# Kernel optimization log

Measured on AMD Instinct MI355X. Metric: run time of the kernel, lower is better.

The kernel has to match this reference:

```python
import jax, jax.numpy as jnp
import numpy as np

HIDDEN = 1024
HEADS = 16
HEAD_DIM = HIDDEN // HEADS
B, T = 4, 2048


def setup_inputs() -> dict:
    key = jax.random.key(0)
    k_x, k_w1, k_b1, k_w2, k_b2 = jax.random.split(key, 5)
    lim1 = 1.0 / np.sqrt(HIDDEN)
    x = jax.random.normal(k_x, (B, T, HIDDEN), dtype=jnp.float32)
    # causal lower-triangular mask, broadcastable to [B, H, T, T]
    mask = jnp.tril(jnp.ones((T, T), dtype=jnp.int32))[None, None, :, :]
    # qkv_proj: Linear(HIDDEN, 3*HIDDEN); torch Linear: y = x @ W.T + b
    W_qkv = jax.random.uniform(k_w1, (3 * HIDDEN, HIDDEN), minval=-lim1, maxval=lim1, dtype=jnp.float32)
    b_qkv = jax.random.uniform(k_b1, (3 * HIDDEN,), minval=-lim1, maxval=lim1, dtype=jnp.float32)
    W_out = jax.random.uniform(k_w2, (HIDDEN, HIDDEN), minval=-lim1, maxval=lim1, dtype=jnp.float32)
    b_out = jax.random.uniform(k_b2, (HIDDEN,), minval=-lim1, maxval=lim1, dtype=jnp.float32)
    return {"x": x, "mask": mask, "W_qkv": W_qkv, "b_qkv": b_qkv, "W_out": W_out, "b_out": b_out}


def reference(x, mask, W_qkv, b_qkv, W_out, b_out):
    Bx, Tx, C = x.shape
    qkv = x @ W_qkv.T + b_qkv                      # [B, T, 3C]
    qkv = qkv.reshape(Bx, Tx, 3, HEADS, HEAD_DIM)
    qkv = jnp.transpose(qkv, (2, 0, 3, 1, 4))      # [3, B, H, T, Dh]
    Q, K, V = qkv[0], qkv[1], qkv[2]
    scale = 1.0 / np.sqrt(HEAD_DIM)
    scores = jnp.einsum('bhqd,bhkd->bhqk', Q, K) * scale  # [B, H, T, T]
    scores = jnp.where(mask == 0, -jnp.inf, scores)
    probs = jax.nn.softmax(scores, axis=-1)
    ctx = jnp.einsum('bhqk,bhkd->bhqd', probs, V)  # [B, H, T, Dh]
    ctx = jnp.transpose(ctx, (0, 2, 1, 3)).reshape(Bx, Tx, C)
    return ctx @ W_out.T + b_out
```

## Files before the change

### kernel.cpp

```cpp
#include <hip/hip_runtime.h>
#include <cstdint>
#include <cstddef>

#define B_ 4
#define T_ 2048
#define C_ 1024
#define H_ 16
#define D_ 64

typedef __attribute__((ext_vector_type(8))) __bf16 bf16x8;
typedef __attribute__((ext_vector_type(4))) float floatx4;

#define QSCL (0.125f * 1.44269504088896f)
#define FMAX 24.0f

__device__ __forceinline__ unsigned short f2bf(float f) {
  union { float f; unsigned int u; } v; v.f = f;
  unsigned int r = v.u + 0x7fffu + ((v.u >> 16) & 1u);
  return (unsigned short)(r >> 16);
}
__device__ __forceinline__ ushort4 pk4(float a, float b, float c, float d) {
  ushort4 u; u.x = f2bf(a); u.y = f2bf(b); u.z = f2bf(c); u.w = f2bf(d);
  return u;
}
__device__ __forceinline__ bf16x8 cvt8(float4 a, float4 b) {
  bf16x8 r;
  r[0] = a.x; r[1] = a.y; r[2] = a.z; r[3] = a.w;
  r[4] = b.x; r[5] = b.y; r[6] = b.z; r[7] = b.w;
  return r;
}
__device__ __forceinline__ unsigned pkbf2(float a, float b) {
  union { __bf16 h[2]; unsigned u; } w;
  w.h[0] = (__bf16)a; w.h[1] = (__bf16)b;
  return w.u;
}

__device__ __forceinline__ void gl_lds16(const void* g, void* l) {
  __builtin_amdgcn_global_load_lds(
      (const __attribute__((address_space(1))) unsigned int*)g,
      (__attribute__((address_space(3))) unsigned int*)l, 16, 0, 0);
}

__global__ __launch_bounds__(256)
void conv_bf16(const float* __restrict__ src, unsigned short* __restrict__ dst,
               int n8) {
  for (int i = blockIdx.x * 256 + threadIdx.x; i < n8; i += gridDim.x * 256) {
    const float4* s = (const float4*)src + 2 * (size_t)i;
    float4 a = s[0], b = s[1];
    ((bf16x8*)dst)[i] = cvt8(a, b);
  }
}

__global__ __launch_bounds__(256)
void conv_tri(const float* __restrict__ s1, unsigned short* __restrict__ d1, int n1,
              const float* __restrict__ s2, unsigned short* __restrict__ d2, int n2,
              const float* __restrict__ s3, unsigned short* __restrict__ d3, int n3) {
  for (int i = blockIdx.x * 256 + threadIdx.x; i < n1 + n2 + n3; i += gridDim.x * 256) {
    const float4* sp; bf16x8* dp;
    if (i < n1)           { sp = (const float4*)s1 + 2 * (size_t)i;       dp = (bf16x8*)d1 + i; }
    else if (i < n1 + n2) { int j = i - n1;      sp = (const float4*)s2 + 2 * (size_t)j; dp = (bf16x8*)d2 + j; }
    else                  { int j = i - n1 - n2; sp = (const float4*)s3 + 2 * (size_t)j; dp = (bf16x8*)d3 + j; }
    float4 a = sp[0], b = sp[1];
    *dp = cvt8(a, b);
  }
}

template<int EPI, int GATHER, int WBF>
__global__ __launch_bounds__(256, 3)
void gemm_bt(const unsigned short* __restrict__ Abf,
             const void* __restrict__ Wraw,
             const float* __restrict__ bias,
             float* __restrict__ out,
             unsigned short* __restrict__ qws,
             unsigned short* __restrict__ kws,
             unsigned short* __restrict__ vtws)
{
  alignas(16) __shared__ unsigned short As[128 * 64];
  alignas(16) __shared__ unsigned short Bs[WBF ? 128 * 64 : 128 * 72];
  const int tid  = threadIdx.x;
  const int lane = tid & 63;
  const int wid  = tid >> 6;
  const int col  = lane & 15;
  const int quad = lane >> 4;
  const int wm = (wid >> 1) << 6;
  const int wn = (wid & 1) << 6;
  const int bm = blockIdx.y << 7;
  const int bn = blockIdx.x << 7;

  const float* Wf          = (const float*)Wraw;
  const unsigned short* Wb = (const unsigned short*)Wraw;

  const int r0 = tid >> 3;
  const int c0 = tid & 7;

  floatx4 acc[4][4];
#pragma unroll
  for (int i = 0; i < 4; ++i)
#pragma unroll
    for (int j = 0; j < 4; ++j)
      acc[i][j] = (floatx4){0.f, 0.f, 0.f, 0.f};

  for (int k0 = 0; k0 < 1024; k0 += 64) {
    __syncthreads();
#pragma unroll
    for (int s = 0; s < 4; ++s) {
      const int row  = (s << 5) + r0;
      const int colE = ((c0 ^ (row & 7)) << 3);
      const unsigned short* gsrc;
      if (GATHER) {
        const int m = bm + row;
        const int b = m >> 11, t = m & 2047;
        const int h = k0 >> 6;
        gsrc = Abf + ((((size_t)(b * 16 + h) << 11) + t) << 6) + colE;
      } else {
        gsrc = Abf + (size_t)(bm + row) * 1024 + k0 + colE;
      }
      gl_lds16(gsrc, (char*)As + (s << 12) + (wid << 10));
    }
    if (WBF) {
#pragma unroll
      for (int s = 0; s < 4; ++s) {
        const int row  = (s << 5) + r0;
        const int colE = ((c0 ^ (row & 7)) << 3);
        const unsigned short* gsrc = Wb + (size_t)(bn + row) * 1024 + k0 + colE;
        gl_lds16(gsrc, (char*)Bs + (s << 12) + (wid << 10));
      }
    } else {
#pragma unroll
      for (int s = 0; s < 4; ++s) {
        const int row = (s << 5) + r0;
        const int kc  = c0 << 3;
        const float* wsrc = &Wf[(size_t)(bn + row) * 1024 + k0 + kc];
        float4 w0 = *(const float4*)wsrc;
        float4 w1 = *(const float4*)(wsrc + 4);
        *(bf16x8*)&Bs[row * 72 + kc] = cvt8(w0, w1);
      }
    }
    __syncthreads();
#pragma unroll
    for (int kk = 0; kk < 64; kk += 32) {
      bf16x8 af[4], bfr[4];
#pragma unroll
      for (int i = 0; i < 4; ++i) {
        const int r = wm + i * 16 + col;
        af[i] = *(const bf16x8*)&As[(r << 6) + ((kk + quad * 8) ^ ((r & 7) << 3))];
      }
#pragma unroll
      for (int j = 0; j < 4; ++j) {
        const int r = wn + j * 16 + col;
        if (WBF)
          bfr[j] = *(const bf16x8*)&Bs[(r << 6) + ((kk + quad * 8) ^ ((r & 7) << 3))];
        else
          bfr[j] = *(const bf16x8*)&Bs[r * 72 + kk + quad * 8];
      }
#pragma unroll
      for (int i = 0; i < 4; ++i)
#pragma unroll
        for (int j = 0; j < 4; ++j)
          acc[i][j] = __builtin_amdgcn_mfma_f32_16x16x32_bf16(af[i], bfr[j], acc[i][j], 0, 0, 0);
    }
  }

#pragma unroll
  for (int i = 0; i < 4; ++i) {
    const int row = bm + wm + i * 16 + quad * 4;
#pragma unroll
    for (int j = 0; j < 4; ++j) {
      const int n  = bn + wn + j * 16 + col;
      const float bv = bias[n];
      float v[4];
#pragma unroll
      for (int r = 0; r < 4; ++r) v[r] = acc[i][j][r] + bv;

      if (EPI == 1) {
#pragma unroll
        for (int r = 0; r < 4; ++r)
          out[(size_t)(row + r) * 1024 + n] = v[r];
      } else {
        const int s   = n >> 10;
        const int rem = n & 1023;
        const int h   = rem >> 6;
        const int d   = rem & 63;
        const int b   = row >> 11;
        const int t   = row & 2047;
        const size_t bh = (size_t)(b * H_ + h);
        if (s == 0) {
#pragma unroll
          for (int r = 0; r < 4; ++r)
            qws[(bh * T_ + t + r) * D_ + d] = f2bf(v[r] * QSCL);
        } else if (s == 1) {
#pragma unroll
          for (int r = 0; r < 4; ++r)
            kws[(bh * T_ + t + r) * D_ + d] = f2bf(v[r]);
        } else {
          *(ushort4*)&vtws[(bh * D_ + d) * T_ + t] = pk4(v[0], v[1], v[2], v[3]);
        }
      }
    }
  }
}

__global__ __launch_bounds__(256, 2)
void attn_causal(unsigned short* __restrict__ qws,
                 const unsigned short* __restrict__ kws,
                 const unsigned short* __restrict__ vtws)
{
  alignas(16) __shared__ unsigned short Ks[2][64 * 64];
  alignas(16) __shared__ unsigned short Vs[2][64 * 64];
  const int tid  = threadIdx.x;
  const int lane = tid & 63;
  const int wid  = tid >> 6;
  const int col  = lane & 15;
  const int quad = lane >> 4;

  const int bh   = blockIdx.x & 63;
  const int band = 15 - (blockIdx.x >> 6);

  const unsigned short* Kp  = kws + (size_t)bh * T_ * D_;
  const unsigned short* Vtp = vtws + (size_t)bh * D_ * T_;

  bf16x8 vones;
#pragma unroll
  for (int i = 0; i < 8; ++i) vones[i] = (__bf16)1.0f;

  const int srow8 = lane >> 3;
  const int swz   = ((lane & 7) ^ srow8) << 3;

#define STAGE(kt_, b_)                                                        \
  do {                                                                        \
    _Pragma("unroll") for (int c2 = 0; c2 < 2; ++c2) {                        \
      const int cb = wid + (c2 << 2);                   \
      gl_lds16(Kp + ((size_t)(((kt_) << 6) + (cb << 3) + srow8) << 6) + swz,  \
               (char*)&Ks[b_][0] + (cb << 10));                               \
      gl_lds16(Vtp + ((size_t)((cb << 3) + srow8) << 11) + ((kt_) << 6) + swz,\
               (char*)&Vs[b_][0] + (cb << 10));                               \
    }                                                                         \
  } while (0)

  const int nk = (band << 1) + 2;
  const int q0 = (band << 7) + (wid << 5);
  unsigned short* Qp = qws + ((size_t)bh * T_ + q0) * D_;

  bf16x8 bq[2][2];
#pragma unroll
  for (int h = 0; h < 2; ++h) {
    bq[h][0] = *(const bf16x8*)&Qp[(h * 16 + col) * D_ + quad * 8];
    bq[h][1] = *(const bf16x8*)&Qp[(h * 16 + col) * D_ + 32 + quad * 8];
  }

  floatx4 o[2][4], ol[2];
#pragma unroll
  for (int h = 0; h < 2; ++h) {
    ol[h] = (floatx4){0.f, 0.f, 0.f, 0.f};
#pragma unroll
    for (int j = 0; j < 4; ++j) o[h][j] = (floatx4){0.f, 0.f, 0.f, 0.f};
  }

  STAGE(0, 0);
  __syncthreads();

  for (int kt = 0; kt < nk; ++kt) {
    const int buf = kt & 1;
    if (kt + 1 < nk) STAGE(kt + 1, buf ^ 1);

    const unsigned short* Kb = &Ks[buf][0];
    bf16x8 kA[4], kB[4];
#pragma unroll
    for (int g = 0; g < 4; ++g) {
      const int r = g * 16 + col;
      kA[g] = *(const bf16x8*)&Kb[(r << 6) + ((quad ^ (col & 7)) << 3)];
      kB[g] = *(const bf16x8*)&Kb[(r << 6) + (((quad | 4) ^ (col & 7)) << 3)];
    }

    floatx4 s[2][4];
    __builtin_amdgcn_s_setprio(1);
#pragma unroll
    for (int h = 0; h < 2; ++h)
#pragma unroll
      for (int g = 0; g < 4; ++g) {
        s[h][g] = (floatx4){-FMAX, -FMAX, -FMAX, -FMAX};
        s[h][g] = __builtin_amdgcn_mfma_f32_16x16x32_bf16(kA[g], bq[h][0], s[h][g], 0, 0, 0);
        s[h][g] = __builtin_amdgcn_mfma_f32_16x16x32_bf16(kB[g], bq[h][1], s[h][g], 0, 0, 0);
      }
    __builtin_amdgcn_s_setprio(0);

    const unsigned short* Vb = &Vs[buf][0];
    bf16x8 vA[4], vB[4];
#pragma unroll
    for (int j = 0; j < 4; ++j) {
      const int r = j * 16 + col;
      vA[j] = *(const bf16x8*)&Vb[(r << 6) + ((quad ^ (col & 7)) << 3)];
      vB[j] = *(const bf16x8*)&Vb[(r << 6) + (((quad | 4) ^ (col & 7)) << 3)];
    }

    if (kt >= nk - 2) {
#pragma unroll
      for (int h = 0; h < 2; ++h) {
        const int lim = q0 - (kt << 6) + (h << 4) + col;
#pragma unroll
        for (int g = 0; g < 4; ++g)
#pragma unroll
          for (int r = 0; r < 4; ++r)
            if (g * 16 + quad * 4 + r > lim) s[h][g][r] = -1e30f;
      }
    }

#pragma unroll
    for (int h = 0; h < 2; ++h)
#pragma unroll
      for (int g = 0; g < 4; ++g)
#pragma unroll
        for (int r = 0; r < 4; ++r)
          s[h][g][r] = __builtin_amdgcn_exp2f(s[h][g][r]);

    __builtin_amdgcn_s_setprio(1);
#pragma unroll
    for (int h = 0; h < 2; ++h) {
      unsigned dw[4][2];
#pragma unroll
      for (int g = 0; g < 4; ++g) {
        dw[g][0] = pkbf2(s[h][g][0], s[h][g][1]);
        dw[g][1] = pkbf2(s[h][g][2], s[h][g][3]);
      }
      unsigned aw[4], bw[4];
      {
        auto t = __builtin_amdgcn_permlane32_swap(dw[0][0], dw[1][0], false, false);
        auto u = __builtin_amdgcn_permlane16_swap(t[0], t[1], false, false);
        aw[0] = u[0]; aw[2] = u[1];
      }
      {
        auto t = __builtin_amdgcn_permlane32_swap(dw[0][1], dw[1][1], false, false);
        auto u = __builtin_amdgcn_permlane16_swap(t[0], t[1], false, false);
        aw[1] = u[0]; aw[3] = u[1];
      }
      {
        auto t = __builtin_amdgcn_permlane32_swap(dw[2][0], dw[3][0], false, false);
        auto u = __builtin_amdgcn_permlane16_swap(t[0], t[1], false, false);
        bw[0] = u[0]; bw[2] = u[1];
      }
      {
        auto t = __builtin_amdgcn_permlane32_swap(dw[2][1], dw[3][1], false, false);
        auto u = __builtin_amdgcn_permlane16_swap(t[0], t[1], false, false);
        bw[1] = u[0]; bw[3] = u[1];
      }
      union { unsigned u[4]; bf16x8 v; } pa0, pa1;
#pragma unroll
      for (int w = 0; w < 4; ++w) { pa0.u[w] = aw[w]; pa1.u[w] = bw[w]; }

#pragma unroll
      for (int j = 0; j < 4; ++j) {
        o[h][j] = __builtin_amdgcn_mfma_f32_16x16x32_bf16(pa0.v, vA[j], o[h][j], 0, 0, 0);
        o[h][j] = __builtin_amdgcn_mfma_f32_16x16x32_bf16(pa1.v, vB[j], o[h][j], 0, 0, 0);
      }
      ol[h] = __builtin_amdgcn_mfma_f32_16x16x32_bf16(pa0.v, vones, ol[h], 0, 0, 0);
      ol[h] = __builtin_amdgcn_mfma_f32_16x16x32_bf16(pa1.v, vones, ol[h], 0, 0, 0);
    }
    __builtin_amdgcn_s_setprio(0);

    __syncthreads();
  }

#pragma unroll
  for (int h = 0; h < 2; ++h) {
    float lr[4];
#pragma unroll
    for (int r = 0; r < 4; ++r) lr[r] = 1.0f / ol[h][r];
#pragma unroll
    for (int j = 0; j < 4; ++j)
#pragma unroll
      for (int r = 0; r < 4; ++r)
        Qp[(size_t)(h * 16 + quad * 4 + r) * D_ + j * 16 + col] =
            f2bf(o[h][j][r] * lr[r]);
  }
#undef STAGE
}

extern "C" void kernel_launch(void* const* d_in, const int* in_sizes, int n_in,
                              void* d_out, int out_size, void* d_ws, size_t ws_size,
                              hipStream_t stream) {
  const float* x     = (const float*)d_in[0];
  const float* W_qkv = (const float*)d_in[2];
  const float* b_qkv = (const float*)d_in[3];
  const float* W_out = (const float*)d_in[4];
  const float* b_out = (const float*)d_in[5];
  float* out = (float*)d_out;

  const size_t per = (size_t)B_ * H_ * T_ * D_;
  unsigned short* qws  = (unsigned short*)d_ws;
  unsigned short* vtws = qws + per;
  unsigned short* kws  = (unsigned short*)d_out;
  unsigned short* xbf  = kws + per;

  const bool bigws  = ws_size >= (size_t)38 * 1024 * 1024;
  const bool hugews = ws_size >= (size_t)40 * 1024 * 1024;
  unsigned short* wqbf = vtws + per;
  unsigned short* wobf = wqbf + (size_t)3 * C_ * C_;

  if (hugews) {
    conv_tri<<<dim3(2048), 256, 0, stream>>>(
        x, xbf, (int)(per >> 3),
        W_qkv, wqbf, (3 * C_ * C_) >> 3,
        W_out, wobf, (C_ * C_) >> 3);
    gemm_bt<0, 0, 1><<<dim3(3072 / 128, 8192 / 128), 256, 0, stream>>>(
        xbf, (const void*)wqbf, b_qkv, nullptr, qws, kws, vtws);
  } else if (bigws) {
    conv_tri<<<dim3(2048), 256, 0, stream>>>(
        x, xbf, (int)(per >> 3),
        W_qkv, wqbf, (3 * C_ * C_) >> 3,
        nullptr, nullptr, 0);
    gemm_bt<0, 0, 1><<<dim3(3072 / 128, 8192 / 128), 256, 0, stream>>>(
        xbf, (const void*)wqbf, b_qkv, nullptr, qws, kws, vtws);
  } else {
    conv_bf16<<<dim3(2048), 256, 0, stream>>>(x, xbf, (int)(per >> 3));
    gemm_bt<0, 0, 0><<<dim3(3072 / 128, 8192 / 128), 256, 0, stream>>>(
        xbf, (const void*)W_qkv, b_qkv, nullptr, qws, kws, vtws);
  }

  attn_causal<<<dim3(16 * 64), 256, 0, stream>>>(qws, kws, vtws);

  if (hugews) {
    gemm_bt<1, 1, 1><<<dim3(1024 / 128, 8192 / 128), 256, 0, stream>>>(
        qws, (const void*)wobf, b_out, out, nullptr, nullptr, nullptr);
  } else {
    conv_bf16<<<dim3(512), 256, 0, stream>>>(W_out, vtws, (C_ * C_) >> 3);
    gemm_bt<1, 1, 1><<<dim3(1024 / 128, 8192 / 128), 256, 0, stream>>>(
        qws, (const void*)vtws, b_out, out, nullptr, nullptr, nullptr);
  }
}
```

Before: 245.0 us.

## Double-buffer LDS tiles in gemm_bt to overlap global loads with MFMA

Doubles the shared-memory A and B tiles and prefetches the next K tile into the alternate buffer while MFMAs run on the current one, which removes one barrier per iteration. The aim is to hide global-to-LDS load latency behind compute in the QKV and output projection GEMMs. LDS use per block doubles, so the launch bound drops from 3 to 2 blocks per CU, trading occupancy for overlap.

After: 247.3 us. About the same (+0.9%).

```diff
diff --git a/kernel.cpp b/kernel.cpp
--- a/kernel.cpp
+++ b/kernel.cpp
@@ -66,7 +66,7 @@
 }
 
 template<int EPI, int GATHER, int WBF>
-__global__ __launch_bounds__(256, 3)
+__global__ __launch_bounds__(256, 2)
 void gemm_bt(const unsigned short* __restrict__ Abf,
              const void* __restrict__ Wraw,
              const float* __restrict__ bias,
@@ -75,8 +75,8 @@
              unsigned short* __restrict__ kws,
              unsigned short* __restrict__ vtws)
 {
-  alignas(16) __shared__ unsigned short As[128 * 64];
-  alignas(16) __shared__ unsigned short Bs[WBF ? 128 * 64 : 128 * 72];
+  alignas(16) __shared__ unsigned short As[2][128 * 64];
+  alignas(16) __shared__ unsigned short Bs[2][WBF ? 128 * 64 : 128 * 72];
   const int tid  = threadIdx.x;
   const int lane = tid & 63;
   const int wid  = tid >> 6;
@@ -100,58 +100,56 @@
     for (int j = 0; j < 4; ++j)
       acc[i][j] = (floatx4){0.f, 0.f, 0.f, 0.f};
 
-  for (int k0 = 0; k0 < 1024; k0 += 64) {
-    __syncthreads();
-#pragma unroll
-    for (int s = 0; s < 4; ++s) {
-      const int row  = (s << 5) + r0;
-      const int colE = ((c0 ^ (row & 7)) << 3);
-      const unsigned short* gsrc;
-      if (GATHER) {
-        const int m = bm + row;
-        const int b = m >> 11, t = m & 2047;
-        const int h = k0 >> 6;
-        gsrc = Abf + ((((size_t)(b * 16 + h) << 11) + t) << 6) + colE;
-      } else {
-        gsrc = Abf + (size_t)(bm + row) * 1024 + k0 + colE;
-      }
-      gl_lds16(gsrc, (char*)As + (s << 12) + (wid << 10));
-    }
-    if (WBF) {
-#pragma unroll
-      for (int s = 0; s < 4; ++s) {
-        const int row  = (s << 5) + r0;
-        const int colE = ((c0 ^ (row & 7)) << 3);
-        const unsigned short* gsrc = Wb + (size_t)(bn + row) * 1024 + k0 + colE;
-        gl_lds16(gsrc, (char*)Bs + (s << 12) + (wid << 10));
-      }
-    } else {
-#pragma unroll
-      for (int s = 0; s < 4; ++s) {
-        const int row = (s << 5) + r0;
-        const int kc  = c0 << 3;
-        const float* wsrc = &Wf[(size_t)(bn + row) * 1024 + k0 + kc];
-        float4 w0 = *(const float4*)wsrc;
-        float4 w1 = *(const float4*)(wsrc + 4);
-        *(bf16x8*)&Bs[row * 72 + kc] = cvt8(w0, w1);
-      }
-    }
-    __syncthreads();
+#define GSTAGE(k0_, nb_)                                                      \
+  do {                                                                        \
+    _Pragma("unroll") for (int s = 0; s < 4; ++s) {                           \
+      const int row  = (s << 5) + r0;                             \
+      const int colE = ((c0 ^ (row & 7)) << 3);             \
+      const unsigned short* gsrc;                                             \
+      if (GATHER) {                                                           \
+        const int m = bm + row;                                               \
+        const int b = m >> 11, t = m & 2047;                                  \
+        const int hh = (k0_) >> 6;                        \
+        gsrc = Abf + ((((size_t)(b * 16 + hh) << 11) + t) << 6) + colE;       \
+      } else {                                                                \
+        gsrc = Abf + (size_t)(bm + row) * 1024 + (k0_) + colE;                \
+      }                                                                       \
+      gl_lds16(gsrc, (char*)&As[nb_][0] + (s << 12) + (wid << 10));           \
+      if (WBF) {                                                              \
+        const unsigned short* ws2 = Wb + (size_t)(bn + row) * 1024 + (k0_) + colE; \
+        gl_lds16(ws2, (char*)&Bs[nb_][0] + (s << 12) + (wid << 10));          \
+      } else {                                                                \
+        const int kc = c0 << 3;                                               \
+        const float* wsrc = &Wf[(size_t)(bn + row) * 1024 + (k0_) + kc];      \
+        float4 w0 = *(const float4*)wsrc;                                     \
+        float4 w1 = *(const float4*)(wsrc + 4);                               \
+        *(bf16x8*)&Bs[nb_][row * 72 + kc] = cvt8(w0, w1);                     \
+      }                                                                       \
+    }                                                                         \
+  } while (0)
+
+  GSTAGE(0, 0);
+  __syncthreads();
+
+  for (int kt = 0; kt < 16; ++kt) {
+    const int buf = kt & 1;
+    if (kt + 1 < 16) GSTAGE((kt + 1) << 6, buf ^ 1);
+
 #pragma unroll
     for (int kk = 0; kk < 64; kk += 32) {
       bf16x8 af[4], bfr[4];
 #pragma unroll
       for (int i = 0; i < 4; ++i) {
         const int r = wm + i * 16 + col;
-        af[i] = *(const bf16x8*)&As[(r << 6) + ((kk + quad * 8) ^ ((r & 7) << 3))];
+        af[i] = *(const bf16x8*)&As[buf][(r << 6) + ((kk + quad * 8) ^ ((r & 7) << 3))];
       }
 #pragma unroll
       for (int j = 0; j < 4; ++j) {
         const int r = wn + j * 16 + col;
         if (WBF)
-          bfr[j] = *(const bf16x8*)&Bs[(r << 6) + ((kk + quad * 8) ^ ((r & 7) << 3))];
+          bfr[j] = *(const bf16x8*)&Bs[buf][(r << 6) + ((kk + quad * 8) ^ ((r & 7) << 3))];
         else
-          bfr[j] = *(const bf16x8*)&Bs[r * 72 + kk + quad * 8];
+          bfr[j] = *(const bf16x8*)&Bs[buf][r * 72 + kk + quad * 8];
       }
 #pragma unroll
       for (int i = 0; i < 4; ++i)
@@ -159,7 +157,10 @@
         for (int j = 0; j < 4; ++j)
           acc[i][j] = __builtin_amdgcn_mfma_f32_16x16x32_bf16(af[i], bfr[j], acc[i][j], 0, 0, 0);
     }
-  }
+
+    __syncthreads();
+  }
+#undef GSTAGE
 
 #pragma unroll
   for (int i = 0; i < 4; ++i) {
```
